# Kernel optimization log

Hardware: AMD Instinct MI355X
Metric: run time of the kernel (lower is better)

The kernel has to match this reference:

```python
import jax, jax.numpy as jnp
import numpy as np

N0, N1, N2 = 400000, 100000, 25000   # nodes per scale (finest -> coarsest)
E0, E1, E2 = 1600000, 400000, 100000
HID, OUT = 64, 2
STATIC_D, DYN_D = 6, 10
K = 3  # filter-matrix polynomial order
NUM_SCALES = 3


def setup_inputs() -> dict:
    key = jax.random.key(0)
    ks = jax.random.split(key, 20)
    def nrm(k, shape, scale=1.0):
        return jax.random.normal(k, shape, dtype=jnp.float32) * scale
    Ntot = N0 + N1 + N2
    inp = {}
    inp["static_features"] = nrm(ks[0], (Ntot, STATIC_D))
    inp["dynamic_features"] = nrm(ks[1], (Ntot, DYN_D))
    Es, Ns = [E0, E1, E2], [N0, N1, N2]
    for i in range(NUM_SCALES):
        inp[f"edge_index{i}"] = jax.random.randint(ks[2 + i], (2, Es[i]), 0, Ns[i], dtype=jnp.int32)
        inp[f"edge_attr{i}"] = jax.random.uniform(ks[5 + i], (Es[i],), dtype=jnp.float32)
    inp["pool_idx1"] = jax.random.randint(ks[8], (N1,), 0, N0, dtype=jnp.int32)
    inp["pool_idx2"] = jax.random.randint(ks[9], (N2,), 0, N0, dtype=jnp.int32)
    fin = STATIC_D + DYN_D
    inp["enc_W1"] = nrm(ks[10], (fin, HID), 1.0 / np.sqrt(fin))
    inp["enc_b1"] = jnp.zeros((HID,), jnp.float32)
    inp["enc_W2"] = nrm(ks[11], (HID, HID), 1.0 / np.sqrt(HID))
    inp["enc_b2"] = jnp.zeros((HID,), jnp.float32)
    inp["enc_prelu"] = jnp.float32(0.25)
    inp["gcn_W"] = nrm(ks[12], (NUM_SCALES, HID, HID), 1.0 / np.sqrt(HID))
    inp["gcn_b"] = jnp.zeros((NUM_SCALES, HID), jnp.float32)
    inp["filter_matrix"] = jnp.ones((NUM_SCALES, K), jnp.float32)
    inp["dec_W1"] = nrm(ks[13], (HID, HID), 1.0 / np.sqrt(HID))
    inp["dec_b1"] = jnp.zeros((HID,), jnp.float32)
    inp["dec_W2"] = nrm(ks[14], (HID, OUT), 1.0 / np.sqrt(HID))
    inp["dec_b2"] = jnp.zeros((OUT,), jnp.float32)
    inp["dec_prelu"] = jnp.float32(0.25)
    return inp


def prelu(x, a):
    return jnp.where(x > 0, x, a * x)


def gcn_conv(x, W, b, src, dst, ew, n):
    # PyG GCNConv: linear, then symmetric-normalized propagation with self loops (weight 1), then bias.
    h = x @ W
    deg = jnp.zeros((n,), x.dtype).at[dst].add(ew) + 1.0  # +1 for self loop
    dinv = jax.lax.rsqrt(deg)
    norm = dinv[src] * ew * dinv[dst]                      # [E]
    out = jnp.zeros_like(h).at[dst].add(norm[:, None] * h[src])
    out = out + h * (dinv * dinv)[:, None]                 # self-loop term: 1/deg
    return out + b


def scatter_mean(x, idx, n):
    cnt = jnp.zeros((n,), x.dtype).at[idx].add(1.0)
    s = jnp.zeros((n, x.shape[1]), x.dtype).at[idx].add(x)
    return s / jnp.maximum(cnt, 1.0)[:, None]


def reference(static_features, dynamic_features, edge_index0, edge_attr0,
              edge_index1, edge_attr1, edge_index2, edge_attr2,
              pool_idx1, pool_idx2,
              enc_W1, enc_b1, enc_W2, enc_b2, enc_prelu,
              gcn_W, gcn_b, filter_matrix,
              dec_W1, dec_b1, dec_W2, dec_b2, dec_prelu):
    # Encoder MLP (prelu after every layer, shared prelu param per MLP)
    x = jnp.concatenate([static_features, dynamic_features], -1)
    x = prelu(x @ enc_W1 + enc_b1, enc_prelu)
    x = prelu(x @ enc_W2 + enc_b2, enc_prelu)

    # Split into scales (node_ptr is static)
    ptr = [0, N0, N0 + N1, N0 + N1 + N2]
    xs = [x[ptr[i]:ptr[i + 1]] for i in range(NUM_SCALES)]
    eis = [edge_index0, edge_index1, edge_index2]
    eas = [edge_attr0, edge_attr1, edge_attr2]
    Ns = [N0, N1, N2]

    # MSGNN layers: K repeated (conv -> tanh), mixed by filter_matrix
    outs = []
    for i in range(NUM_SCALES):
        src, dst = eis[i][0], eis[i][1]
        h = xs[i]
        acc = jnp.zeros_like(h)
        for k in range(K):
            h = jnp.tanh(gcn_conv(h, gcn_W[i], gcn_b[i], src, dst, eas[i], Ns[i]))
            acc = acc + filter_matrix[i, k] * h
        outs.append(acc)

    # Skip-connection pooling: scatter-mean coarse scales onto finest scale
    fin = outs[0]
    fin = fin + scatter_mean(outs[1], pool_idx1, N0)
    fin = fin + scatter_mean(outs[2], pool_idx2, N0)

    # Decoder MLP
    y = prelu(fin @ dec_W1 + dec_b1, dec_prelu)
    y = prelu(y @ dec_W2 + dec_b2, dec_prelu)
    return y
```

## Files before the change

kernel.cpp:

```cpp
#include <hip/hip_runtime.h>
#include <hip/hip_bf16.h>

typedef __hip_bfloat16 bf16;
typedef short  bf16x8  __attribute__((ext_vector_type(8)));
typedef __bf16 bf16x8n __attribute__((ext_vector_type(8)));
typedef float  f32x4   __attribute__((ext_vector_type(4)));
typedef unsigned long long u64;

constexpr int cN0 = 400000, cN1 = 100000, cN2 = 25000;
constexpr int cNTOT = cN0 + cN1 + cN2;
constexpr int cE0 = 1600000, cE1 = 400000, cE2 = 100000;

static __device__ __forceinline__ float b2f(bf16 x) { return __bfloat162float(x); }
static __device__ __forceinline__ float bflo(unsigned u) { return __uint_as_float(u << 16); }
static __device__ __forceinline__ float bfhi(unsigned u) { return __uint_as_float(u & 0xffff0000u); }

static __device__ __forceinline__ short f2bf_rtne(float f) {
    unsigned u = __float_as_uint(f);
    u = (u + 0x7fffu + ((u >> 16) & 1u)) >> 16;
    return (short)u;
}
static __device__ __forceinline__ void split2(float x, short& h, short& l) {
    unsigned u = __float_as_uint(x);
    h = (short)(u >> 16);
    l = f2bf_rtne(x - __uint_as_float(u & 0xffff0000u));
}

static __device__ __forceinline__ f32x4 mfma16(bf16x8 a, bf16x8 b, f32x4 c) {
    return __builtin_amdgcn_mfma_f32_16x16x32_bf16((bf16x8n)a, (bf16x8n)b, c, 0, 0, 0);
}

static __device__ __forceinline__ void pack_a8(const float* s8, bf16x8& ah, bf16x8& al) {
    float4 v0 = ((const float4*)s8)[0];
    float4 v1 = ((const float4*)s8)[1];
    float xx[8] = {v0.x, v0.y, v0.z, v0.w, v1.x, v1.y, v1.z, v1.w};
#pragma unroll
    for (int j = 0; j < 8; j++) { short h, l; split2(xx[j], h, l); ah[j] = h; al[j] = l; }
}

static __device__ __forceinline__ void pack_b8(const float* __restrict__ W, int ldn,
                                               int kbase, int col, int kmax,
                                               bf16x8& bh, bf16x8& bl) {
#pragma unroll
    for (int j = 0; j < 8; j++) {
        int k = kbase + j;
        float w = (k < kmax) ? W[(size_t)k * ldn + col] : 0.f;
        short h, l; split2(w, h, l); bh[j] = h; bl[j] = l;
    }
}

__global__ __launch_bounds__(256, 2)
void enc_kernel(const float* __restrict__ stat, const float* __restrict__ dyn,
                const float* __restrict__ W1, const float* __restrict__ b1,
                const float* __restrict__ W2, const float* __restrict__ b2,
                const float* __restrict__ pa, bf16* __restrict__ X, int nn)
{
    __shared__ float sF[4][16 * 20];
    __shared__ float sH[4][16 * 68];
    const int lane = threadIdx.x & 63;
    const int slot = threadIdx.x >> 6;
    const int r = lane & 15, g4 = lane >> 4;
    const int wid = blockIdx.x * (blockDim.x >> 6) + slot;
    const int nw  = gridDim.x * (blockDim.x >> 6);

    bf16x8 B1h[4], B1l[4], B2h[2][4], B2l[2][4];
#pragma unroll
    for (int nb = 0; nb < 4; nb++)
        pack_b8(W1, 64, g4 * 8, nb * 16 + r, 16, B1h[nb], B1l[nb]);
#pragma unroll
    for (int s = 0; s < 2; s++)
#pragma unroll
        for (int nb = 0; nb < 4; nb++)
            pack_b8(W2, 64, s * 32 + g4 * 8, nb * 16 + r, 64, B2h[s][nb], B2l[s][nb]);
    float bc1[4], bc2[4];
#pragma unroll
    for (int nb = 0; nb < 4; nb++) { bc1[nb] = b1[nb * 16 + r]; bc2[nb] = b2[nb * 16 + r]; }
    const float a = pa[0];
    float* F = sF[slot];
    float* H = sH[slot];
    const int ntile = (nn + 15) >> 4;

    for (int tt = wid; tt < ntile; tt += nw) {
        const int n0 = tt << 4;
        const int nv = min(16, nn - n0);
        for (int t = lane; t < nv * 6; t += 64)
            F[(t / 6) * 20 + (t % 6)] = stat[(size_t)n0 * 6 + t];
        for (int t = lane; t < nv * 10; t += 64)
            F[(t / 10) * 20 + 6 + (t % 10)] = dyn[(size_t)n0 * 10 + t];
        __builtin_amdgcn_wave_barrier();

        f32x4 C1[4];
#pragma unroll
        for (int nb = 0; nb < 4; nb++) C1[nb] = (f32x4){bc1[nb], bc1[nb], bc1[nb], bc1[nb]};
        bf16x8 ah, al;
        if (g4 < 2) pack_a8(F + r * 20 + g4 * 8, ah, al);
        else        { ah = (bf16x8)(short)0; al = (bf16x8)(short)0; }
#pragma unroll
        for (int nb = 0; nb < 4; nb++) {
            C1[nb] = mfma16(ah, B1h[nb], C1[nb]);
            C1[nb] = mfma16(ah, B1l[nb], C1[nb]);
            C1[nb] = mfma16(al, B1h[nb], C1[nb]);
        }
#pragma unroll
        for (int nb = 0; nb < 4; nb++)
#pragma unroll
            for (int q = 0; q < 4; q++) {
                float v = C1[nb][q];
                v = v > 0.f ? v : a * v;
                H[(g4 * 4 + q) * 68 + nb * 16 + r] = v;
            }
        __builtin_amdgcn_wave_barrier();

        f32x4 C2[4];
#pragma unroll
        for (int nb = 0; nb < 4; nb++) C2[nb] = (f32x4){bc2[nb], bc2[nb], bc2[nb], bc2[nb]};
#pragma unroll
        for (int s = 0; s < 2; s++) {
            bf16x8 a2h, a2l;
            pack_a8(H + r * 68 + s * 32 + g4 * 8, a2h, a2l);
#pragma unroll
            for (int nb = 0; nb < 4; nb++) {
                C2[nb] = mfma16(a2h, B2h[s][nb], C2[nb]);
                C2[nb] = mfma16(a2h, B2l[s][nb], C2[nb]);
                C2[nb] = mfma16(a2l, B2h[s][nb], C2[nb]);
            }
        }
#pragma unroll
        for (int nb = 0; nb < 4; nb++)
#pragma unroll
            for (int q = 0; q < 4; q++) {
                float v = C2[nb][q];
                v = v > 0.f ? v : a * v;
                const int row = g4 * 4 + q;
                if (row < nv)
                    X[(size_t)(n0 + row) * 64 + nb * 16 + r] = __float2bfloat16(v);
            }
        __builtin_amdgcn_wave_barrier();
    }
}

__global__ void zdc_kernel(u64* p, int n)
{
    int t = blockIdx.x * 256 + threadIdx.x;
    if (t < n) p[t] = 0ull;
}
__global__ void edge_pack_kernel(const int* __restrict__ dst, const float* __restrict__ ew,
                                 u64* __restrict__ dc, int ne)
{
    int e = blockIdx.x * 256 + threadIdx.x;
    if (e < ne) {
        u64 pk = (1ull << 40) | (u64)(ew[e] * 268435456.f + 0.5f);
        atomicAdd(&dc[dst[e]], pk);
    }
}

__global__ void scan_blk_kernel(const u64* __restrict__ dc, int* __restrict__ base,
                                int* __restrict__ bsum, float* __restrict__ dinv, int n)
{
    __shared__ int s[256];
    const int tid = threadIdx.x;
    const int t = blockIdx.x * 256 + tid;
    u64 pk = (t < n) ? dc[t] : 0ull;
    int v = (int)(pk >> 40);
    s[tid] = v;
    __syncthreads();
#pragma unroll
    for (int d = 1; d < 256; d <<= 1) {
        int u = (tid >= d) ? s[tid - d] : 0;
        __syncthreads();
        s[tid] += u;
        __syncthreads();
    }
    if (t < n) {
        base[t] = s[tid] - v;
        const float deg = 1.f + (float)(pk & ((1ull << 40) - 1ull)) * (1.f / 268435456.f);
        dinv[t] = rsqrtf(deg);
    }
    if (tid == 255) bsum[blockIdx.x] = s[255];
}
__global__ void scan_top_kernel(int* __restrict__ bsum, int nb)
{
    __shared__ int s[256];
    __shared__ int carry;
    const int tid = threadIdx.x;
    if (tid == 0) carry = 0;
    __syncthreads();
    for (int c0 = 0; c0 < nb; c0 += 256) {
        const int t = c0 + tid;
        int v = (t < nb) ? bsum[t] : 0;
        s[tid] = v;
        __syncthreads();
#pragma unroll
        for (int d = 1; d < 256; d <<= 1) {
            int u = (tid >= d) ? s[tid - d] : 0;
            __syncthreads();
            s[tid] += u;
            __syncthreads();
        }
        if (t < nb) bsum[t] = carry + s[tid] - v;
        __syncthreads();
        if (tid == 255) carry += s[255];
        __syncthreads();
    }
}
__global__ void scan_add_kernel(int* __restrict__ base, const int* __restrict__ bsum,
                                int* __restrict__ cur, int n)
{
    const int t = blockIdx.x * 256 + threadIdx.x;
    if (t < n) { int b = base[t] + bsum[blockIdx.x]; base[t] = b; cur[t] = b; }
}

__global__ void grab_kernel(const int* __restrict__ cnt, int* __restrict__ base,
                            int* __restrict__ cur, int* __restrict__ gc, int n)
{
    int t = blockIdx.x * 256 + threadIdx.x;
    if (t < n) { int b = atomicAdd(gc, cnt[t]); base[t] = b; cur[t] = b; }
}
__global__ void fill_edge_kernel(const int* __restrict__ src, const int* __restrict__ dst,
                                 const float* __restrict__ ew, const float* __restrict__ dinv,
                                 int* __restrict__ cur, int* __restrict__ srcp,
                                 bf16* __restrict__ normp, int ne)
{
    int e = blockIdx.x * 256 + threadIdx.x;
    if (e >= ne) return;
    int d = dst[e], s = src[e];
    int pos = atomicAdd(&cur[d], 1);
    srcp[pos]  = s;
    normp[pos] = __float2bfloat16(dinv[s] * ew[e] * dinv[d]);
}
__global__ void zint2_kernel(int* __restrict__ p, int* __restrict__ gc, int n)
{
    int t = blockIdx.x * 256 + threadIdx.x;
    if (t < n) p[t] = 0;
    if (t == 0) gc[0] = 0;
}
__global__ void cnt_idx_kernel(const int* __restrict__ idx, int* __restrict__ cnt, int n)
{
    int j = blockIdx.x * 256 + threadIdx.x;
    if (j < n) atomicAdd(&cnt[idx[j]], 1);
}
__global__ void fill_idx_kernel(const int* __restrict__ idx, int* __restrict__ cur,
                                int* __restrict__ jp, int n)
{
    int j = blockIdx.x * 256 + threadIdx.x;
    if (j >= n) return;
    int pos = atomicAdd(&cur[idx[j]], 1);
    jp[pos] = j;
}

__global__ __launch_bounds__(256, 3)
void fused_conv_kernel(const int* __restrict__ base,
                       const int* __restrict__ srcp, const bf16* __restrict__ normp,
                       const bf16* __restrict__ h_in, bf16* __restrict__ h_out,
                       const float* __restrict__ dinv,
                       const float* __restrict__ W, int woff,
                       const float* __restrict__ bias, int boff,
                       const float* __restrict__ filt, int foff,
                       int first, int store_h, float* __restrict__ acc,
                       int nn, int ne)
{
    __shared__ float sb[4][16 * 68];
    const int lane = threadIdx.x & 63;
    const int slot = threadIdx.x >> 6;
    const int r = lane & 15, g4 = lane >> 4;
    const int wid  = blockIdx.x * (blockDim.x >> 6) + slot;
    const int nw   = gridDim.x * (blockDim.x >> 6);

    bf16x8 Bh[2][4], Bl[2][4];
#pragma unroll
    for (int s = 0; s < 2; s++)
#pragma unroll
        for (int nb = 0; nb < 4; nb++)
            pack_b8(W + woff, 64, s * 32 + g4 * 8, nb * 16 + r, 64, Bh[s][nb], Bl[s][nb]);
    float bc[4];
#pragma unroll
    for (int nb = 0; nb < 4; nb++) bc[nb] = bias[boff + nb * 16 + r];
    const float fc = filt[foff];
    float* sbrow = sb[slot];
    const int ngrp = (nn + 15) >> 4;

    for (int grp = wid; grp < ngrp; grp += nw) {
        const int n0 = grp << 4;
        int rpl = 0;
        if (lane <= 16) rpl = (n0 + lane < nn) ? base[n0 + lane] : ne;
        const int b4 = g4 << 2;
        const int q0 = __shfl(rpl, b4);
        const int q1 = __shfl(rpl, b4 + 1);
        const int q2 = __shfl(rpl, b4 + 2);
        const int q3 = __shfl(rpl, b4 + 3);
        const int q4 = __shfl(rpl, b4 + 4);

        int   curl  = 0;
        int   rnext = q1;
        float g0 = 0.f, g1 = 0.f, g2 = 0.f, g3 = 0.f;
        auto flush = [&]() {
            *(float4*)(sbrow + (b4 + curl) * 68 + (r << 2)) = make_float4(g0, g1, g2, g3);
            g0 = g1 = g2 = g3 = 0.f;
            curl++;
            rnext = (curl == 1) ? q2 : (curl == 2) ? q3 : (curl == 3) ? q4 : 0x7fffffff;
        };

        for (int eb = q0; eb < q4; eb += 16) {
            const int ei_ = min(eb + r, q4 - 1);
            int   sv = srcp[ei_];
            float nv = (eb + r < q4) ? b2f(normp[ei_]) : 0.f;
#pragma unroll
            for (int t = 0; t < 16; t += 4) {
                const int bidx = (g4 << 4) + t;
                int   s0 = __shfl(sv, bidx),     s1 = __shfl(sv, bidx + 1);
                int   s2 = __shfl(sv, bidx + 2), s3 = __shfl(sv, bidx + 3);
                float m0 = __shfl(nv, bidx),     m1 = __shfl(nv, bidx + 1);
                float m2 = __shfl(nv, bidx + 2), m3 = __shfl(nv, bidx + 3);
                uint2 p0 = *(const uint2*)(h_in + ((size_t)s0 << 6) + (r << 2));
                uint2 p1 = *(const uint2*)(h_in + ((size_t)s1 << 6) + (r << 2));
                uint2 p2 = *(const uint2*)(h_in + ((size_t)s2 << 6) + (r << 2));
                uint2 p3 = *(const uint2*)(h_in + ((size_t)s3 << 6) + (r << 2));
                while (eb + t     >= rnext) flush();
                g0 += m0 * bflo(p0.x); g1 += m0 * bfhi(p0.x);
                g2 += m0 * bflo(p0.y); g3 += m0 * bfhi(p0.y);
                while (eb + t + 1 >= rnext) flush();
                g0 += m1 * bflo(p1.x); g1 += m1 * bfhi(p1.x);
                g2 += m1 * bflo(p1.y); g3 += m1 * bfhi(p1.y);
                while (eb + t + 2 >= rnext) flush();
                g0 += m2 * bflo(p2.x); g1 += m2 * bfhi(p2.x);
                g2 += m2 * bflo(p2.y); g3 += m2 * bfhi(p2.y);
                while (eb + t + 3 >= rnext) flush();
                g0 += m3 * bflo(p3.x); g1 += m3 * bfhi(p3.x);
                g2 += m3 * bflo(p3.y); g3 += m3 * bfhi(p3.y);
            }
        }
        while (curl < 4) flush();
        __builtin_amdgcn_wave_barrier();

        {
            const int node = n0 + r;
            const int ncl = min(node, nn - 1);
            float di = dinv[ncl];
            di = (node < nn) ? di * di : 0.f;
            float* rowp = sbrow + r * 68 + (g4 << 4);
#pragma unroll
            for (int hh = 0; hh < 2; hh++) {
                uint4 hv = *(const uint4*)(h_in + ((size_t)ncl << 6) + (g4 << 4) + hh * 8);
                float4 f0 = *(float4*)(rowp + hh * 8);
                float4 f1 = *(float4*)(rowp + hh * 8 + 4);
                f0.x += di * bflo(hv.x); f0.y += di * bfhi(hv.x);
                f0.z += di * bflo(hv.y); f0.w += di * bfhi(hv.y);
                f1.x += di * bflo(hv.z); f1.y += di * bfhi(hv.z);
                f1.z += di * bflo(hv.w); f1.w += di * bfhi(hv.w);
                *(float4*)(rowp + hh * 8)     = f0;
                *(float4*)(rowp + hh * 8 + 4) = f1;
            }
        }
        __builtin_amdgcn_wave_barrier();

        const int nv16 = min(16, nn - n0);
        f32x4 C[4];
#pragma unroll
        for (int nb = 0; nb < 4; nb++) C[nb] = (f32x4){bc[nb], bc[nb], bc[nb], bc[nb]};
#pragma unroll
        for (int s = 0; s < 2; s++) {
            bf16x8 ah, al;
            pack_a8(sbrow + r * 68 + s * 32 + g4 * 8, ah, al);
#pragma unroll
            for (int nb = 0; nb < 4; nb++) {
                C[nb] = mfma16(ah, Bh[s][nb], C[nb]);
                C[nb] = mfma16(ah, Bl[s][nb], C[nb]);
                C[nb] = mfma16(al, Bh[s][nb], C[nb]);
            }
        }
#pragma unroll
        for (int nb = 0; nb < 4; nb++)
#pragma unroll
            for (int q = 0; q < 4; q++) {
                const int row = g4 * 4 + q;
                if (row < nv16) {
                    const float sv_ = C[nb][q];
                    const float e = __expf(2.f * sv_);
                    const float h = 1.f - 2.f * __builtin_amdgcn_rcpf(e + 1.f);
                    const size_t ai = (size_t)(n0 + row) * 64 + nb * 16 + r;
                    if (store_h) h_out[ai] = __float2bfloat16(h);
                    acc[ai] = (first ? 0.f : acc[ai]) + fc * h;
                }
            }
        __builtin_amdgcn_wave_barrier();
    }
}

__global__ void pool_gather_kernel(const int* __restrict__ base, const int* __restrict__ cnt,
                                   const int* __restrict__ jp, const float* __restrict__ accc,
                                   float* __restrict__ fin, int nn)
{
    const int lane = threadIdx.x & 63;
    const int n = blockIdx.x * (blockDim.x >> 6) + (threadIdx.x >> 6);
    if (n >= nn) return;
    const int m = cnt[n];
    if (m == 0) return;
    const int bs = base[n];
    float s = 0.f;
    for (int t = bs; t < bs + m; t++) {
        int j = jp[t];
        s += accc[(size_t)j * 64 + lane];
    }
    fin[(size_t)n * 64 + lane] += s / (float)m;
}

__global__ __launch_bounds__(256, 3)
void dec_kernel(const float* __restrict__ fin,
                const float* __restrict__ W1, const float* __restrict__ b1,
                const float* __restrict__ W2, const float* __restrict__ b2,
                const float* __restrict__ pa, float* __restrict__ out, int nn)
{
    const int lane = threadIdx.x & 63;
    const int r = lane & 15, g4 = lane >> 4;
    const int wid = blockIdx.x * (blockDim.x >> 6) + (threadIdx.x >> 6);
    const int nw  = gridDim.x * (blockDim.x >> 6);

    bf16x8 Wh[2][4], Wl[2][4];
#pragma unroll
    for (int s = 0; s < 2; s++)
#pragma unroll
        for (int nb = 0; nb < 4; nb++)
            pack_b8(W1, 64, s * 32 + g4 * 8, nb * 16 + r, 64, Wh[s][nb], Wl[s][nb]);
    float bc[4], w20[4], w21[4];
#pragma unroll
    for (int nb = 0; nb < 4; nb++) {
        bc[nb]  = b1[nb * 16 + r];
        w20[nb] = W2[(nb * 16 + r) * 2 + 0];
        w21[nb] = W2[(nb * 16 + r) * 2 + 1];
    }
    const float bb20 = b2[0], bb21 = b2[1];
    const float a = pa[0];
    const int ntile = (nn + 15) >> 4;

    for (int tt = wid; tt < ntile; tt += nw) {
        const int n0 = tt << 4;
        f32x4 C[4];
#pragma unroll
        for (int nb = 0; nb < 4; nb++) C[nb] = (f32x4){bc[nb], bc[nb], bc[nb], bc[nb]};
#pragma unroll
        for (int s = 0; s < 2; s++) {
            bf16x8 ah, al;
            pack_a8(fin + (size_t)(n0 + r) * 64 + s * 32 + g4 * 8, ah, al);
#pragma unroll
            for (int nb = 0; nb < 4; nb++) {
                C[nb] = mfma16(ah, Wh[s][nb], C[nb]);
                C[nb] = mfma16(ah, Wl[s][nb], C[nb]);
                C[nb] = mfma16(al, Wh[s][nb], C[nb]);
            }
        }
#pragma unroll
        for (int q = 0; q < 4; q++) {
            float p0 = 0.f, p1 = 0.f;
#pragma unroll
            for (int nb = 0; nb < 4; nb++) {
                float y = C[nb][q];
                y = y > 0.f ? y : a * y;
                p0 += y * w20[nb]; p1 += y * w21[nb];
            }
            p0 += __shfl_xor(p0, 1); p1 += __shfl_xor(p1, 1);
            p0 += __shfl_xor(p0, 2); p1 += __shfl_xor(p1, 2);
            p0 += __shfl_xor(p0, 4); p1 += __shfl_xor(p1, 4);
            p0 += __shfl_xor(p0, 8); p1 += __shfl_xor(p1, 8);
            if (r == 0) {
                const int node = n0 + g4 * 4 + q;
                if (node < nn) {
                    float o0 = p0 + bb20; o0 = o0 > 0.f ? o0 : a * o0;
                    float o1 = p1 + bb21; o1 = o1 > 0.f ? o1 : a * o1;
                    ((float2*)out)[node] = make_float2(o0, o1);
                }
            }
        }
    }
}

extern "C" void kernel_launch(void* const* d_in, const int* in_sizes, int n_in,
                              void* d_out, int out_size, void* d_ws, size_t ws_size,
                              hipStream_t stream)
{
    const float* stat = (const float*)d_in[0];
    const float* dyn  = (const float*)d_in[1];
    const int*   ei[3]   = {(const int*)d_in[2], (const int*)d_in[4], (const int*)d_in[6]};
    const float* ea[3]   = {(const float*)d_in[3], (const float*)d_in[5], (const float*)d_in[7]};
    const int*   pidx[2] = {(const int*)d_in[8], (const int*)d_in[9]};
    const float* encW1 = (const float*)d_in[10]; const float* encb1 = (const float*)d_in[11];
    const float* encW2 = (const float*)d_in[12]; const float* encb2 = (const float*)d_in[13];
    const float* encpa = (const float*)d_in[14];
    const float* gW    = (const float*)d_in[15]; const float* gbias = (const float*)d_in[16];
    const float* filt  = (const float*)d_in[17];
    const float* dW1   = (const float*)d_in[18]; const float* db1   = (const float*)d_in[19];
    const float* dW2   = (const float*)d_in[20]; const float* db2   = (const float*)d_in[21];
    const float* dpa   = (const float*)d_in[22];

    auto al = [](size_t x) { return (x + 255) & ~(size_t)255; };
    char* w = (char*)d_ws;
    size_t off = 0;
    bf16* X    = (bf16*)(w + off); off += al((size_t)cNTOT * 64 * 2);
    bf16* HB   = (bf16*)(w + off); off += al((size_t)cN0 * 64 * 2);
    float* FIN = (float*)(w + off); off += al((size_t)cN0 * 64 * 4);
    float* ACCC= (float*)(w + off); off += al((size_t)cN1 * 64 * 4);
    float* DINV= (float*)(w + off); off += al((size_t)cN0 * 4);
    int* CNTI  = (int*)(w + off);  off += al((size_t)cN0 * 4);
    int* BASE  = (int*)(w + off);  off += al((size_t)cN0 * 4);
    int* CUR   = (int*)(w + off);  off += al((size_t)cN0 * 4);
    int* SRCP  = (int*)(w + off);  off += al((size_t)cE0 * 4);
    bf16* NORMP= (bf16*)(w + off); off += al((size_t)cE0 * 2);
    int* JP    = (int*)(w + off);  off += al((size_t)cN1 * 4);
    int* GC    = (int*)(w + off);  off += 256;
    int* BSUM  = (int*)(w + off);  off += al((size_t)2048 * 4);
    u64* DC    = (u64*)ACCC;

    const int Ns[3]  = {cN0, cN1, cN2};
    const int Es[3]  = {cE0, cE1, cE2};
    const int ptr[3] = {0, cN0, cN0 + cN1};
#define NB(x) (((x) + 255) / 256)

    enc_kernel<<<4096, 256, 0, stream>>>(stat, dyn, encW1, encb1, encW2, encb2, encpa, X, cNTOT);

    for (int i = 0; i < 3; i++) {
        const int* srcp_in = ei[i];
        const int* dstp    = ei[i] + Es[i];
        zdc_kernel      <<<NB(Ns[i]), 256, 0, stream>>>(DC, Ns[i]);
        edge_pack_kernel<<<NB(Es[i]), 256, 0, stream>>>(dstp, ea[i], DC, Es[i]);
        scan_blk_kernel <<<NB(Ns[i]), 256, 0, stream>>>(DC, BASE, BSUM, DINV, Ns[i]);
        scan_top_kernel <<<1, 256, 0, stream>>>(BSUM, NB(Ns[i]));
        scan_add_kernel <<<NB(Ns[i]), 256, 0, stream>>>(BASE, BSUM, CUR, Ns[i]);
        fill_edge_kernel<<<NB(Es[i]), 256, 0, stream>>>(srcp_in, dstp, ea[i], DINV, CUR, SRCP, NORMP, Es[i]);

        bf16* ping = X + (size_t)ptr[i] * 64;
        bf16* pong = HB;
        float* acc_i = (i == 0) ? FIN : ACCC;
        const int ngrp = (Ns[i] + 15) / 16;
        const int cblk = min(4096, (ngrp + 3) / 4);
        for (int k = 0; k < 3; k++) {
            bf16* hin  = (k & 1) ? pong : ping;
            bf16* hout = (k & 1) ? ping : pong;
            fused_conv_kernel<<<cblk, 256, 0, stream>>>(BASE, SRCP, NORMP,
                hin, hout, DINV, gW, i * 4096, gbias, i * 64,
                filt, i * 3 + k, (k == 0) ? 1 : 0, (k < 2) ? 1 : 0, acc_i, Ns[i], Es[i]);
        }
        if (i >= 1) {
            int nj = (i == 1) ? cN1 : cN2;
            const int* pp = pidx[i - 1];
            zint2_kernel   <<<NB(cN0), 256, 0, stream>>>(CNTI, GC, cN0);
            cnt_idx_kernel <<<NB(nj), 256, 0, stream>>>(pp, CNTI, nj);
            grab_kernel    <<<NB(cN0), 256, 0, stream>>>(CNTI, BASE, CUR, GC, cN0);
            fill_idx_kernel<<<NB(nj), 256, 0, stream>>>(pp, CUR, JP, nj);
            pool_gather_kernel<<<(cN0 + 3) / 4, 256, 0, stream>>>(BASE, CNTI, JP, ACCC, FIN, cN0);
        }
    }
    dec_kernel<<<4096, 256, 0, stream>>>(FIN, dW1, db1, dW2, db2, dpa, (float*)d_out, cN0);
#undef NB
}
```

Baseline: 1.307 ms.

## Stage MFMA weight fragments in LDS and widen gather batch to eight

Moves the split bf16 hi/lo weight fragments from per-lane registers into shared memory, built once per block, to free VGPRs. Raises launch bounds from 3 to 4 blocks per CU. The edge gather loop now issues 8 row loads before accumulating instead of 4, increasing memory-level parallelism. In exchange it adds LDS reads per MFMA group and a block-wide sync, and the padded 65-word stride makes the 128-bit LDS reads unaligned.

```diff
diff --git a/kernel.cpp b/kernel.cpp
--- a/kernel.cpp
+++ b/kernel.cpp
@@ -248,7 +248,7 @@
     jp[pos] = j;
 }
 
-__global__ __launch_bounds__(256, 3)
+__global__ __launch_bounds__(256, 4)
 void fused_conv_kernel(const int* __restrict__ base,
                        const int* __restrict__ srcp, const bf16* __restrict__ normp,
                        const bf16* __restrict__ h_in, bf16* __restrict__ h_out,
@@ -260,23 +260,38 @@
                        int nn, int ne)
 {
     __shared__ float sb[4][16 * 68];
+    __shared__ unsigned sW[64 * 65];
     const int lane = threadIdx.x & 63;
     const int slot = threadIdx.x >> 6;
     const int r = lane & 15, g4 = lane >> 4;
     const int wid  = blockIdx.x * (blockDim.x >> 6) + slot;
     const int nw   = gridDim.x * (blockDim.x >> 6);
 
-    bf16x8 Bh[2][4], Bl[2][4];
-#pragma unroll
-    for (int s = 0; s < 2; s++)
-#pragma unroll
-        for (int nb = 0; nb < 4; nb++)
-            pack_b8(W + woff, 64, s * 32 + g4 * 8, nb * 16 + r, 64, Bh[s][nb], Bl[s][nb]);
+    if (slot == 0) {
+        unsigned* dstw = sW + lane * 65;
+#pragma unroll
+        for (int s = 0; s < 2; s++)
+#pragma unroll
+            for (int nb = 0; nb < 4; nb++) {
+                bf16x8 bh, bl;
+                pack_b8(W + woff, 64, s * 32 + g4 * 8, nb * 16 + r, 64, bh, bl);
+                const int f = s * 4 + nb;
+                uint4 uh = *(uint4*)&bh;
+                uint4 ul = *(uint4*)&bl;
+                dstw[f * 4 + 0] = uh.x; dstw[f * 4 + 1] = uh.y;
+                dstw[f * 4 + 2] = uh.z; dstw[f * 4 + 3] = uh.w;
+                dstw[32 + f * 4 + 0] = ul.x; dstw[32 + f * 4 + 1] = ul.y;
+                dstw[32 + f * 4 + 2] = ul.z; dstw[32 + f * 4 + 3] = ul.w;
+            }
+    }
+    __syncthreads();
+
     float bc[4];
 #pragma unroll
     for (int nb = 0; nb < 4; nb++) bc[nb] = bias[boff + nb * 16 + r];
     const float fc = filt[foff];
     float* sbrow = sb[slot];
+    const unsigned* myW = sW + lane * 65;
     const int ngrp = (nn + 15) >> 4;
 
     for (int grp = wid; grp < ngrp; grp += nw) {
@@ -305,28 +320,23 @@
             int   sv = srcp[ei_];
             float nv = (eb + r < q4) ? b2f(normp[ei_]) : 0.f;
 #pragma unroll
-            for (int t = 0; t < 16; t += 4) {
+            for (int t = 0; t < 16; t += 8) {
                 const int bidx = (g4 << 4) + t;
-                int   s0 = __shfl(sv, bidx),     s1 = __shfl(sv, bidx + 1);
-                int   s2 = __shfl(sv, bidx + 2), s3 = __shfl(sv, bidx + 3);
-                float m0 = __shfl(nv, bidx),     m1 = __shfl(nv, bidx + 1);
-                float m2 = __shfl(nv, bidx + 2), m3 = __shfl(nv, bidx + 3);
-                uint2 p0 = *(const uint2*)(h_in + ((size_t)s0 << 6) + (r << 2));
-                uint2 p1 = *(const uint2*)(h_in + ((size_t)s1 << 6) + (r << 2));
-                uint2 p2 = *(const uint2*)(h_in + ((size_t)s2 << 6) + (r << 2));
-                uint2 p3 = *(const uint2*)(h_in + ((size_t)s3 << 6) + (r << 2));
-                while (eb + t     >= rnext) flush();
-                g0 += m0 * bflo(p0.x); g1 += m0 * bfhi(p0.x);
-                g2 += m0 * bflo(p0.y); g3 += m0 * bfhi(p0.y);
-                while (eb + t + 1 >= rnext) flush();
-                g0 += m1 * bflo(p1.x); g1 += m1 * bfhi(p1.x);
-                g2 += m1 * bflo(p1.y); g3 += m1 * bfhi(p1.y);
-                while (eb + t + 2 >= rnext) flush();
-                g0 += m2 * bflo(p2.x); g1 += m2 * bfhi(p2.x);
-                g2 += m2 * bflo(p2.y); g3 += m2 * bfhi(p2.y);
-                while (eb + t + 3 >= rnext) flush();
-                g0 += m3 * bflo(p3.x); g1 += m3 * bfhi(p3.x);
-                g2 += m3 * bflo(p3.y); g3 += m3 * bfhi(p3.y);
+                int ss[8]; float mm[8]; uint2 pp[8];
+#pragma unroll
+                for (int j = 0; j < 8; j++) {
+                    ss[j] = __shfl(sv, bidx + j);
+                    mm[j] = __shfl(nv, bidx + j);
+                }
+#pragma unroll
+                for (int j = 0; j < 8; j++)
+                    pp[j] = *(const uint2*)(h_in + ((size_t)ss[j] << 6) + (r << 2));
+#pragma unroll
+                for (int j = 0; j < 8; j++) {
+                    while (eb + t + j >= rnext) flush();
+                    g0 += mm[j] * bflo(pp[j].x); g1 += mm[j] * bfhi(pp[j].x);
+                    g2 += mm[j] * bflo(pp[j].y); g3 += mm[j] * bfhi(pp[j].y);
+                }
             }
         }
         while (curl < 4) flush();
@@ -363,9 +373,14 @@
             pack_a8(sbrow + r * 68 + s * 32 + g4 * 8, ah, al);
 #pragma unroll
             for (int nb = 0; nb < 4; nb++) {
-                C[nb] = mfma16(ah, Bh[s][nb], C[nb]);
-                C[nb] = mfma16(ah, Bl[s][nb], C[nb]);
-                C[nb] = mfma16(al, Bh[s][nb], C[nb]);
+                const int f = s * 4 + nb;
+                uint4 uh = *(const uint4*)(myW + f * 4);
+                uint4 ul = *(const uint4*)(myW + 32 + f * 4);
+                bf16x8 bh = *(bf16x8*)&uh;
+                bf16x8 bl = *(bf16x8*)&ul;
+                C[nb] = mfma16(ah, bh, C[nb]);
+                C[nb] = mfma16(ah, bl, C[nb]);
+                C[nb] = mfma16(al, bh, C[nb]);
             }
         }
 #pragma unroll
```

After: 1.262 ms. -3.5%, faster.
